# Kernel optimization log

Hardware: AMD Instinct MI355X
Metric: run time of the kernel (lower is better)

Reference implementation:

```python
import jax, jax.numpy as jnp
import numpy as np

B, H, L = 16, 1024, 4096


def setup_inputs() -> dict:
    key = jax.random.key(0)
    k1, k2 = jax.random.split(key)
    x = jax.random.normal(k1, (B, H, L), dtype=jnp.float32)
    # SSM kernel output k: (channels=1, d_model=H, L)
    k = jax.random.normal(k2, (1, H, L), dtype=jnp.float32) * 0.02
    D = jnp.ones((1, H, 1), dtype=jnp.float32)  # skip-connection scale
    return {"x": x, "k": k, "D": D}


def reference(x, k, D):
    # unidirectional FFT long convolution (S4-style):
    # y = irfft(rfft(x, 2L) * rfft(k, 2L))[..., :L] + x * D
    Lx = x.shape[-1]
    n = 2 * Lx
    k_f = jnp.fft.rfft(k, n=n)          # (1, H, n//2+1) complex
    x_f = jnp.fft.rfft(x, n=n)          # (B, H, n//2+1) complex
    y = jnp.fft.irfft(x_f * k_f, n=n)[..., :Lx]  # (B, H, L)
    return y + x * D
```

## Files before the change

### kernel.cpp

```cpp
#include <hip/hip_runtime.h>

#define LCONV 4096
#define NFFT 8192
#define NT 256
#define HCH 1024
#define BATCH 16
#define PI_F 3.14159265358979f
#define C707 0.70710678118654752f
#define C16A 0.92387953251128674f
#define S16A 0.38268343236508977f

#define SW(i) ((i) ^ (((i) >> 4) & 15))

__device__ __forceinline__ float2 cadd(float2 a, float2 b){ return make_float2(a.x+b.x, a.y+b.y); }
__device__ __forceinline__ float2 csub(float2 a, float2 b){ return make_float2(a.x-b.x, a.y-b.y); }
__device__ __forceinline__ float2 cmul(float2 a, float2 b){ return make_float2(a.x*b.x - a.y*b.y, a.x*b.y + a.y*b.x); }
__device__ __forceinline__ float2 mW81 (float2 d){ return make_float2( C707*(d.x+d.y),  C707*(d.y-d.x)); }
__device__ __forceinline__ float2 mNI  (float2 d){ return make_float2( d.y, -d.x); }
__device__ __forceinline__ float2 mW83 (float2 d){ return make_float2( C707*(d.y-d.x), -C707*(d.x+d.y)); }
__device__ __forceinline__ float2 mW81c(float2 d){ return make_float2( C707*(d.x-d.y),  C707*(d.x+d.y)); }
__device__ __forceinline__ float2 mPI  (float2 d){ return make_float2(-d.y,  d.x); }
__device__ __forceinline__ float2 mW83c(float2 d){ return make_float2(-C707*(d.x+d.y),  C707*(d.x-d.y)); }

__device__ __forceinline__ void net8_fwd(float2 a[8]) {
    float2 t0=cadd(a[0],a[4]), t4=csub(a[0],a[4]);
    float2 t1=cadd(a[1],a[5]), t5=mW81(csub(a[1],a[5]));
    float2 t2=cadd(a[2],a[6]), t6=mNI (csub(a[2],a[6]));
    float2 t3=cadd(a[3],a[7]), t7=mW83(csub(a[3],a[7]));
    float2 u0=cadd(t0,t2), u2=csub(t0,t2);
    float2 u1=cadd(t1,t3), u3=mNI(csub(t1,t3));
    float2 u4=cadd(t4,t6), u6=csub(t4,t6);
    float2 u5=cadd(t5,t7), u7=mNI(csub(t5,t7));
    a[0]=cadd(u0,u1); a[1]=csub(u0,u1);
    a[2]=cadd(u2,u3); a[3]=csub(u2,u3);
    a[4]=cadd(u4,u5); a[5]=csub(u4,u5);
    a[6]=cadd(u6,u7); a[7]=csub(u6,u7);
}
__device__ __forceinline__ void net8_inv(float2 a[8]) {
    float2 t0=cadd(a[0],a[4]), t4=csub(a[0],a[4]);
    float2 t1=cadd(a[1],a[5]), t5=mW81c(csub(a[1],a[5]));
    float2 t2=cadd(a[2],a[6]), t6=mPI  (csub(a[2],a[6]));
    float2 t3=cadd(a[3],a[7]), t7=mW83c(csub(a[3],a[7]));
    float2 u0=cadd(t0,t2), u2=csub(t0,t2);
    float2 u1=cadd(t1,t3), u3=mPI(csub(t1,t3));
    float2 u4=cadd(t4,t6), u6=csub(t4,t6);
    float2 u5=cadd(t5,t7), u7=mPI(csub(t5,t7));
    a[0]=cadd(u0,u1); a[1]=csub(u0,u1);
    a[2]=cadd(u2,u3); a[3]=csub(u2,u3);
    a[4]=cadd(u4,u5); a[5]=csub(u4,u5);
    a[6]=cadd(u6,u7); a[7]=csub(u6,u7);
}

template<int M, bool INV>
__device__ __forceinline__ void bf8(float2* z, int idx, const float2 w[8]) {
    float2 a[8];
    if (!INV) {
#pragma unroll
        for (int q = 0; q < 8; ++q) a[q] = z[SW(idx + q*M)];
        net8_fwd(a);
        z[SW(idx      )] = a[0];
        z[SW(idx + 4*M)] = cmul(a[1], w[4]);
        z[SW(idx + 2*M)] = cmul(a[2], w[2]);
        z[SW(idx + 6*M)] = cmul(a[3], w[6]);
        z[SW(idx + 1*M)] = cmul(a[4], w[1]);
        z[SW(idx + 5*M)] = cmul(a[5], w[5]);
        z[SW(idx + 3*M)] = cmul(a[6], w[3]);
        z[SW(idx + 7*M)] = cmul(a[7], w[7]);
    } else {
        a[0] = z[SW(idx)];
#pragma unroll
        for (int q = 1; q < 8; ++q) a[q] = cmul(z[SW(idx + q*M)], w[q]);
        net8_inv(a);
        z[SW(idx      )] = a[0];
        z[SW(idx + 4*M)] = a[1];
        z[SW(idx + 2*M)] = a[2];
        z[SW(idx + 6*M)] = a[3];
        z[SW(idx + 1*M)] = a[4];
        z[SW(idx + 5*M)] = a[5];
        z[SW(idx + 3*M)] = a[6];
        z[SW(idx + 7*M)] = a[7];
    }
}

template<int M, bool INV>
__device__ __forceinline__ void stage8(float2* z, int tid) {
    __syncthreads();
    const float ang = (INV ? 2.0f : -2.0f) * PI_F / (8.0f * (float)M);
    if (M == 1024) {
        float2 w1, wstep;
        __sincosf(ang * (float)tid, &w1.y, &w1.x);
        __sincosf(ang * 256.0f, &wstep.y, &wstep.x);
#pragma unroll
        for (int s = 0; s < 4; ++s) {
            float2 w[8];
            w[0] = make_float2(1.f, 0.f);
            w[1] = w1;
#pragma unroll
            for (int q = 2; q < 8; ++q) w[q] = cmul(w[q-1], w1);
            bf8<M, INV>(z, tid + 256*s, w);
            w1 = cmul(w1, wstep);
        }
    } else {
        const int LOG2M = (M == 128) ? 7 : 4;
        int j  = tid & (M - 1);
        int g0 = tid >> LOG2M;
        float2 w[8];
        w[0] = make_float2(1.f, 0.f);
        __sincosf(ang * (float)j, &w[1].y, &w[1].x);
#pragma unroll
        for (int q = 2; q < 8; ++q) w[q] = cmul(w[q-1], w[1]);
#pragma unroll
        for (int s = 0; s < 4; ++s) {
            int base = (g0 + (256 / M) * s) * (8 * M);
            bf8<M, INV>(z, base + j, w);
        }
    }
}

template<bool INV>
__device__ __forceinline__ void stage16(float2* z, int tid) {
    __syncthreads();
#pragma unroll
    for (int s = 0; s < 2; ++s) {
        int b = (tid + 256*s) * 16;
        float2 a[16];
#pragma unroll
        for (int e = 0; e < 16; ++e) a[e] = z[SW(b + e)];
        float2 lo[8], hi[8];
#pragma unroll
        for (int i = 0; i < 8; ++i) {
            lo[i] = cadd(a[i], a[i+8]);
            hi[i] = csub(a[i], a[i+8]);
        }
        if (!INV) {
            hi[1] = cmul(hi[1], make_float2( C16A, -S16A));
            hi[2] = mW81(hi[2]);
            hi[3] = cmul(hi[3], make_float2( S16A, -C16A));
            hi[4] = mNI (hi[4]);
            hi[5] = cmul(hi[5], make_float2(-S16A, -C16A));
            hi[6] = mW83(hi[6]);
            hi[7] = cmul(hi[7], make_float2(-C16A, -S16A));
            net8_fwd(lo); net8_fwd(hi);
        } else {
            hi[1] = cmul(hi[1], make_float2( C16A,  S16A));
            hi[2] = mW81c(hi[2]);
            hi[3] = cmul(hi[3], make_float2( S16A,  C16A));
            hi[4] = mPI (hi[4]);
            hi[5] = cmul(hi[5], make_float2(-S16A,  C16A));
            hi[6] = mW83c(hi[6]);
            hi[7] = cmul(hi[7], make_float2(-C16A,  S16A));
            net8_inv(lo); net8_inv(hi);
        }
        const int rev3[8] = {0,4,2,6,1,5,3,7};
#pragma unroll
        for (int s2 = 0; s2 < 8; ++s2) {
            z[SW(b + 2*rev3[s2]    )] = lo[s2];
            z[SW(b + 2*rev3[s2] + 1)] = hi[s2];
        }
    }
}

__global__ __launch_bounds__(NT) void kfft_kernel(const float* __restrict__ k,
                                                  float2* __restrict__ Kf) {
    __shared__ float2 z[NFFT];
    int h = blockIdx.x, tid = threadIdx.x;
    const float* kr = k + (size_t)h * LCONV;
#pragma unroll
    for (int jj = 0; jj < 16; ++jj) {
        int i = tid + NT*jj;
        z[SW(i)]         = make_float2(kr[i], 0.f);
        z[SW(i + LCONV)] = make_float2(0.f, 0.f);
    }
    stage8<1024, false>(z, tid);
    stage8<128,  false>(z, tid);
    stage8<16,   false>(z, tid);
    stage16<false>(z, tid);
    __syncthreads();
    const float invN = 1.0f / (float)NFFT;
    float2* out = Kf + (size_t)h * NFFT;
#pragma unroll
    for (int jj = 0; jj < 32; ++jj) {
        int i = tid + NT*jj;
        float2 v = z[SW(i)];
        out[i] = make_float2(v.x * invN, v.y * invN);
    }
}

__global__ __launch_bounds__(NT) void conv_kernel(const float* __restrict__ x,
                                                  const float2* __restrict__ Kf,
                                                  const float* __restrict__ Dv,
                                                  float* __restrict__ y) {
    __shared__ float2 z[NFFT];
    int bid = blockIdx.x;
    int h = bid >> 3;
    int pb = bid & 7;
    int b0 = pb*2, b1 = pb*2 + 1;
    int tid = threadIdx.x;

    const float* x0 = x + ((size_t)b0 * HCH + h) * LCONV;
    const float* x1 = x + ((size_t)b1 * HCH + h) * LCONV;

    float2 xr[16];
#pragma unroll
    for (int jj = 0; jj < 16; ++jj) {
        int i = tid + NT*jj;
        xr[jj] = make_float2(x0[i], x1[i]);
        z[SW(i)]         = xr[jj];
        z[SW(i + LCONV)] = make_float2(0.f, 0.f);
    }

    stage8<1024, false>(z, tid);
    stage8<128,  false>(z, tid);
    stage8<16,   false>(z, tid);
    stage16<false>(z, tid);

    __syncthreads();
    const float2* kf = Kf + (size_t)h * NFFT;
#pragma unroll
    for (int jj = 0; jj < 32; ++jj) {
        int i = tid + NT*jj;
        z[SW(i)] = cmul(z[SW(i)], kf[i]);
    }

    stage16<true>(z, tid);
    stage8<16,   true>(z, tid);
    stage8<128,  true>(z, tid);
    stage8<1024, true>(z, tid);

    __syncthreads();
    float d = Dv[h];
    float* y0 = y + ((size_t)b0 * HCH + h) * LCONV;
    float* y1 = y + ((size_t)b1 * HCH + h) * LCONV;
#pragma unroll
    for (int jj = 0; jj < 16; ++jj) {
        int i = tid + NT*jj;
        float2 r = z[SW(i)];
        y0[i] = r.x + xr[jj].x * d;
        y1[i] = r.y + xr[jj].y * d;
    }
}

extern "C" void kernel_launch(void* const* d_in, const int* in_sizes, int n_in,
                              void* d_out, int out_size, void* d_ws, size_t ws_size,
                              hipStream_t stream) {
    const float* x  = (const float*)d_in[0];
    const float* k  = (const float*)d_in[1];
    const float* Dv = (const float*)d_in[2];
    float* y  = (float*)d_out;
    float2* Kf = (float2*)d_ws;

    kfft_kernel<<<HCH, NT, 0, stream>>>(k, Kf);
    conv_kernel<<<HCH * (BATCH/2), NT, 0, stream>>>(x, Kf, Dv, y);
}
```

Baseline: 658.9 us.

## Restructure FFT convolution as 16x16x32 decomposition with fused skip term and pruned stages

```diff
diff --git a/kernel.cpp b/kernel.cpp
--- a/kernel.cpp
+++ b/kernel.cpp
@@ -1,28 +1,35 @@
 #include <hip/hip_runtime.h>
 
+
 #define LCONV 4096
-#define NFFT 8192
-#define NT 256
-#define HCH 1024
+#define NFFT  8192
+#define NT    256
+#define HCH   1024
 #define BATCH 16
-#define PI_F 3.14159265358979f
+
 #define C707 0.70710678118654752f
 #define C16A 0.92387953251128674f
 #define S16A 0.38268343236508977f
-
-#define SW(i) ((i) ^ (((i) >> 4) & 15))
-
-__device__ __forceinline__ float2 cadd(float2 a, float2 b){ return make_float2(a.x+b.x, a.y+b.y); }
-__device__ __forceinline__ float2 csub(float2 a, float2 b){ return make_float2(a.x-b.x, a.y-b.y); }
-__device__ __forceinline__ float2 cmul(float2 a, float2 b){ return make_float2(a.x*b.x - a.y*b.y, a.x*b.y + a.y*b.x); }
-__device__ __forceinline__ float2 mW81 (float2 d){ return make_float2( C707*(d.x+d.y),  C707*(d.y-d.x)); }
-__device__ __forceinline__ float2 mNI  (float2 d){ return make_float2( d.y, -d.x); }
-__device__ __forceinline__ float2 mW83 (float2 d){ return make_float2( C707*(d.y-d.x), -C707*(d.x+d.y)); }
-__device__ __forceinline__ float2 mW81c(float2 d){ return make_float2( C707*(d.x-d.y),  C707*(d.x+d.y)); }
-__device__ __forceinline__ float2 mPI  (float2 d){ return make_float2(-d.y,  d.x); }
-__device__ __forceinline__ float2 mW83c(float2 d){ return make_float2(-C707*(d.x+d.y),  C707*(d.x-d.y)); }
-
-__device__ __forceinline__ void net8_fwd(float2 a[8]) {
+#define C32A 0.98078528040323044f
+#define S32A 0.19509032201612827f
+#define C32B 0.83146961230254524f
+#define S32B 0.55557023301960222f
+
+#define A256f  (-0.0245436926061702596f)
+#define A512f  (-0.0122718463030851298f)
+#define A8192f (-7.66990393942820615e-4f)
+
+static __device__ __forceinline__ float2 cadd(float2 a, float2 b){ return make_float2(a.x+b.x, a.y+b.y); }
+static __device__ __forceinline__ float2 csub(float2 a, float2 b){ return make_float2(a.x-b.x, a.y-b.y); }
+static __device__ __forceinline__ float2 cmul(float2 a, float2 b){ return make_float2(a.x*b.x - a.y*b.y, a.x*b.y + a.y*b.x); }
+static __device__ __forceinline__ float2 mW81 (float2 d){ return make_float2( C707*(d.x+d.y),  C707*(d.y-d.x)); }
+static __device__ __forceinline__ float2 mNI  (float2 d){ return make_float2( d.y, -d.x); }
+static __device__ __forceinline__ float2 mW83 (float2 d){ return make_float2( C707*(d.y-d.x), -C707*(d.x+d.y)); }
+static __device__ __forceinline__ float2 mW81c(float2 d){ return make_float2( C707*(d.x-d.y),  C707*(d.x+d.y)); }
+static __device__ __forceinline__ float2 mPI  (float2 d){ return make_float2(-d.y,  d.x); }
+static __device__ __forceinline__ float2 mW83c(float2 d){ return make_float2(-C707*(d.x+d.y),  C707*(d.x-d.y)); }
+
+static __device__ __forceinline__ void net8_fwd(float2 a[8]) {
     float2 t0=cadd(a[0],a[4]), t4=csub(a[0],a[4]);
     float2 t1=cadd(a[1],a[5]), t5=mW81(csub(a[1],a[5]));
     float2 t2=cadd(a[2],a[6]), t6=mNI (csub(a[2],a[6]));
@@ -36,7 +43,7 @@
     a[4]=cadd(u4,u5); a[5]=csub(u4,u5);
     a[6]=cadd(u6,u7); a[7]=csub(u6,u7);
 }
-__device__ __forceinline__ void net8_inv(float2 a[8]) {
+static __device__ __forceinline__ void net8_inv(float2 a[8]) {
     float2 t0=cadd(a[0],a[4]), t4=csub(a[0],a[4]);
     float2 t1=cadd(a[1],a[5]), t5=mW81c(csub(a[1],a[5]));
     float2 t2=cadd(a[2],a[6]), t6=mPI  (csub(a[2],a[6]));
@@ -51,192 +58,340 @@
     a[6]=cadd(u6,u7); a[7]=csub(u6,u7);
 }
 
-template<int M, bool INV>
-__device__ __forceinline__ void bf8(float2* z, int idx, const float2 w[8]) {
-    float2 a[8];
-    if (!INV) {
-#pragma unroll
-        for (int q = 0; q < 8; ++q) a[q] = z[SW(idx + q*M)];
-        net8_fwd(a);
-        z[SW(idx      )] = a[0];
-        z[SW(idx + 4*M)] = cmul(a[1], w[4]);
-        z[SW(idx + 2*M)] = cmul(a[2], w[2]);
-        z[SW(idx + 6*M)] = cmul(a[3], w[6]);
-        z[SW(idx + 1*M)] = cmul(a[4], w[1]);
-        z[SW(idx + 5*M)] = cmul(a[5], w[5]);
-        z[SW(idx + 3*M)] = cmul(a[6], w[3]);
-        z[SW(idx + 7*M)] = cmul(a[7], w[7]);
-    } else {
-        a[0] = z[SW(idx)];
-#pragma unroll
-        for (int q = 1; q < 8; ++q) a[q] = cmul(z[SW(idx + q*M)], w[q]);
-        net8_inv(a);
-        z[SW(idx      )] = a[0];
-        z[SW(idx + 4*M)] = a[1];
-        z[SW(idx + 2*M)] = a[2];
-        z[SW(idx + 6*M)] = a[3];
-        z[SW(idx + 1*M)] = a[4];
-        z[SW(idx + 5*M)] = a[5];
-        z[SW(idx + 3*M)] = a[6];
-        z[SW(idx + 7*M)] = a[7];
-    }
-}
-
-template<int M, bool INV>
-__device__ __forceinline__ void stage8(float2* z, int tid) {
-    __syncthreads();
-    const float ang = (INV ? 2.0f : -2.0f) * PI_F / (8.0f * (float)M);
-    if (M == 1024) {
-        float2 w1, wstep;
-        __sincosf(ang * (float)tid, &w1.y, &w1.x);
-        __sincosf(ang * 256.0f, &wstep.y, &wstep.x);
-#pragma unroll
-        for (int s = 0; s < 4; ++s) {
-            float2 w[8];
-            w[0] = make_float2(1.f, 0.f);
-            w[1] = w1;
-#pragma unroll
-            for (int q = 2; q < 8; ++q) w[q] = cmul(w[q-1], w1);
-            bf8<M, INV>(z, tid + 256*s, w);
-            w1 = cmul(w1, wstep);
-        }
-    } else {
-        const int LOG2M = (M == 128) ? 7 : 4;
-        int j  = tid & (M - 1);
-        int g0 = tid >> LOG2M;
-        float2 w[8];
-        w[0] = make_float2(1.f, 0.f);
-        __sincosf(ang * (float)j, &w[1].y, &w[1].x);
-#pragma unroll
-        for (int q = 2; q < 8; ++q) w[q] = cmul(w[q-1], w[1]);
-#pragma unroll
-        for (int s = 0; s < 4; ++s) {
-            int base = (g0 + (256 / M) * s) * (8 * M);
-            bf8<M, INV>(z, base + j, w);
-        }
-    }
-}
-
-template<bool INV>
-__device__ __forceinline__ void stage16(float2* z, int tid) {
-    __syncthreads();
-#pragma unroll
-    for (int s = 0; s < 2; ++s) {
-        int b = (tid + 256*s) * 16;
-        float2 a[16];
-#pragma unroll
-        for (int e = 0; e < 16; ++e) a[e] = z[SW(b + e)];
-        float2 lo[8], hi[8];
-#pragma unroll
-        for (int i = 0; i < 8; ++i) {
-            lo[i] = cadd(a[i], a[i+8]);
-            hi[i] = csub(a[i], a[i+8]);
-        }
-        if (!INV) {
-            hi[1] = cmul(hi[1], make_float2( C16A, -S16A));
-            hi[2] = mW81(hi[2]);
-            hi[3] = cmul(hi[3], make_float2( S16A, -C16A));
-            hi[4] = mNI (hi[4]);
-            hi[5] = cmul(hi[5], make_float2(-S16A, -C16A));
-            hi[6] = mW83(hi[6]);
-            hi[7] = cmul(hi[7], make_float2(-C16A, -S16A));
-            net8_fwd(lo); net8_fwd(hi);
-        } else {
-            hi[1] = cmul(hi[1], make_float2( C16A,  S16A));
-            hi[2] = mW81c(hi[2]);
-            hi[3] = cmul(hi[3], make_float2( S16A,  C16A));
-            hi[4] = mPI (hi[4]);
-            hi[5] = cmul(hi[5], make_float2(-S16A,  C16A));
-            hi[6] = mW83c(hi[6]);
-            hi[7] = cmul(hi[7], make_float2(-C16A,  S16A));
-            net8_inv(lo); net8_inv(hi);
-        }
-        const int rev3[8] = {0,4,2,6,1,5,3,7};
-#pragma unroll
-        for (int s2 = 0; s2 < 8; ++s2) {
-            z[SW(b + 2*rev3[s2]    )] = lo[s2];
-            z[SW(b + 2*rev3[s2] + 1)] = hi[s2];
-        }
+static __device__ __forceinline__ void fft16_fwd(float2 a[16]) {
+    float2 lo[8], hi[8];
+#pragma unroll
+    for (int n=0;n<8;++n){ lo[n]=cadd(a[n],a[n+8]); hi[n]=csub(a[n],a[n+8]); }
+    hi[1]=cmul(hi[1],make_float2( C16A,-S16A));
+    hi[2]=mW81(hi[2]);
+    hi[3]=cmul(hi[3],make_float2( S16A,-C16A));
+    hi[4]=mNI(hi[4]);
+    hi[5]=cmul(hi[5],make_float2(-S16A,-C16A));
+    hi[6]=mW83(hi[6]);
+    hi[7]=cmul(hi[7],make_float2(-C16A,-S16A));
+    net8_fwd(lo); net8_fwd(hi);
+#pragma unroll
+    for (int s=0;s<8;++s){ a[s]=lo[s]; a[8+s]=hi[s]; }
+}
+static __device__ __forceinline__ void fft16_inv_nat(float2 a[16]) {
+    float2 lo[8], hi[8];
+#pragma unroll
+    for (int n=0;n<8;++n){ lo[n]=cadd(a[n],a[n+8]); hi[n]=csub(a[n],a[n+8]); }
+    hi[1]=cmul(hi[1],make_float2( C16A, S16A));
+    hi[2]=mW81c(hi[2]);
+    hi[3]=cmul(hi[3],make_float2( S16A, C16A));
+    hi[4]=mPI(hi[4]);
+    hi[5]=cmul(hi[5],make_float2(-S16A, C16A));
+    hi[6]=mW83c(hi[6]);
+    hi[7]=cmul(hi[7],make_float2(-C16A, S16A));
+    net8_inv(lo); net8_inv(hi);
+#pragma unroll
+    for (int s=0;s<8;++s){ a[s]=lo[s]; a[8+s]=hi[s]; }
+}
+static __device__ __forceinline__ void fft32_fwd(float2 a[32]) {
+    float2 lo[16], hi[16];
+#pragma unroll
+    for (int n=0;n<16;++n){ lo[n]=cadd(a[n],a[n+16]); hi[n]=csub(a[n],a[n+16]); }
+    hi[ 1]=cmul(hi[ 1],make_float2( C32A,-S32A));
+    hi[ 2]=cmul(hi[ 2],make_float2( C16A,-S16A));
+    hi[ 3]=cmul(hi[ 3],make_float2( C32B,-S32B));
+    hi[ 4]=mW81(hi[ 4]);
+    hi[ 5]=cmul(hi[ 5],make_float2( S32B,-C32B));
+    hi[ 6]=cmul(hi[ 6],make_float2( S16A,-C16A));
+    hi[ 7]=cmul(hi[ 7],make_float2( S32A,-C32A));
+    hi[ 8]=mNI(hi[ 8]);
+    hi[ 9]=cmul(hi[ 9],make_float2(-S32A,-C32A));
+    hi[10]=cmul(hi[10],make_float2(-S16A,-C16A));
+    hi[11]=cmul(hi[11],make_float2(-S32B,-C32B));
+    hi[12]=mW83(hi[12]);
+    hi[13]=cmul(hi[13],make_float2(-C32B,-S32B));
+    hi[14]=cmul(hi[14],make_float2(-C16A,-S16A));
+    hi[15]=cmul(hi[15],make_float2(-C32A,-S32A));
+    fft16_fwd(lo); fft16_fwd(hi);
+#pragma unroll
+    for (int s=0;s<16;++s){ a[s]=lo[s]; a[16+s]=hi[s]; }
+}
+
+static __device__ __forceinline__ void inv8_r2n(const float2 b[8], float2 o[8]) {
+    float2 e0=cadd(b[0],b[1]), e1=csub(b[0],b[1]);
+    float2 f0=cadd(b[2],b[3]), f1=mPI(csub(b[2],b[3]));
+    float2 E0=cadd(e0,f0), E2=csub(e0,f0);
+    float2 E1=cadd(e1,f1), E3=csub(e1,f1);
+    float2 g0=cadd(b[4],b[5]), g1=csub(b[4],b[5]);
+    float2 h0=cadd(b[6],b[7]), h1=mPI(csub(b[6],b[7]));
+    float2 O0=cadd(g0,h0), O2=csub(g0,h0);
+    float2 O1=cadd(g1,h1), O3=csub(g1,h1);
+    float2 T0=O0, T1=mW81c(O1), T2=mPI(O2), T3=mW83c(O3);
+    o[0]=cadd(E0,T0); o[4]=csub(E0,T0);
+    o[1]=cadd(E1,T1); o[5]=csub(E1,T1);
+    o[2]=cadd(E2,T2); o[6]=csub(E2,T2);
+    o[3]=cadd(E3,T3); o[7]=csub(E3,T3);
+}
+static __device__ __forceinline__ void inv16_r2n(const float2 a[16], float2 o[16]) {
+    float2 E[8], O[8];
+    inv8_r2n(a, E); inv8_r2n(a+8, O);
+    float2 T[8];
+    T[0]=O[0];
+    T[1]=cmul(O[1],make_float2( C16A, S16A));
+    T[2]=mW81c(O[2]);
+    T[3]=cmul(O[3],make_float2( S16A, C16A));
+    T[4]=mPI(O[4]);
+    T[5]=cmul(O[5],make_float2(-S16A, C16A));
+    T[6]=mW83c(O[6]);
+    T[7]=cmul(O[7],make_float2(-C16A, S16A));
+#pragma unroll
+    for (int n=0;n<8;++n){ o[n]=cadd(E[n],T[n]); o[n+8]=csub(E[n],T[n]); }
+}
+static __device__ __forceinline__ void inv32_r2n(const float2 a[32], float2 o[32]) {
+    float2 E[16], O[16], T;
+    inv16_r2n(a, E); inv16_r2n(a+16, O);
+    T=O[0];                                  o[ 0]=cadd(E[ 0],T); o[16]=csub(E[ 0],T);
+    T=cmul(O[ 1],make_float2( C32A, S32A)); o[ 1]=cadd(E[ 1],T); o[17]=csub(E[ 1],T);
+    T=cmul(O[ 2],make_float2( C16A, S16A)); o[ 2]=cadd(E[ 2],T); o[18]=csub(E[ 2],T);
+    T=cmul(O[ 3],make_float2( C32B, S32B)); o[ 3]=cadd(E[ 3],T); o[19]=csub(E[ 3],T);
+    T=mW81c(O[ 4]);                          o[ 4]=cadd(E[ 4],T); o[20]=csub(E[ 4],T);
+    T=cmul(O[ 5],make_float2( S32B, C32B)); o[ 5]=cadd(E[ 5],T); o[21]=csub(E[ 5],T);
+    T=cmul(O[ 6],make_float2( S16A, C16A)); o[ 6]=cadd(E[ 6],T); o[22]=csub(E[ 6],T);
+    T=cmul(O[ 7],make_float2( S32A, C32A)); o[ 7]=cadd(E[ 7],T); o[23]=csub(E[ 7],T);
+    T=mPI(O[ 8]);                            o[ 8]=cadd(E[ 8],T); o[24]=csub(E[ 8],T);
+    T=cmul(O[ 9],make_float2(-S32A, C32A)); o[ 9]=cadd(E[ 9],T); o[25]=csub(E[ 9],T);
+    T=cmul(O[10],make_float2(-S16A, C16A)); o[10]=cadd(E[10],T); o[26]=csub(E[10],T);
+    T=cmul(O[11],make_float2(-S32B, C32B)); o[11]=cadd(E[11],T); o[27]=csub(E[11],T);
+    T=mW83c(O[12]);                          o[12]=cadd(E[12],T); o[28]=csub(E[12],T);
+    T=cmul(O[13],make_float2(-C32B, S32B)); o[13]=cadd(E[13],T); o[29]=csub(E[13],T);
+    T=cmul(O[14],make_float2(-C16A, S16A)); o[14]=cadd(E[14],T); o[30]=csub(E[14],T);
+    T=cmul(O[15],make_float2(-C32A, S32A)); o[15]=cadd(E[15],T); o[31]=csub(E[15],T);
+}
+
+static __device__ __forceinline__ void f1_stage(float2* __restrict__ z, const float2 d[8],
+                                                int n2, int col)
+{
+    constexpr int rev3[8] = {0,4,2,6,1,5,3,7};
+    float2 lo[8], hi[8];
+    lo[0]=d[0]; hi[0]=d[0];
+    lo[1]=d[1]; hi[1]=cmul(d[1],make_float2( C16A,-S16A));
+    lo[2]=d[2]; hi[2]=mW81(d[2]);
+    lo[3]=d[3]; hi[3]=cmul(d[3],make_float2( S16A,-C16A));
+    lo[4]=d[4]; hi[4]=mNI(d[4]);
+    lo[5]=d[5]; hi[5]=cmul(d[5],make_float2(-S16A,-C16A));
+    lo[6]=d[6]; hi[6]=mW83(d[6]);
+    lo[7]=d[7]; hi[7]=cmul(d[7],make_float2(-C16A,-S16A));
+    net8_fwd(lo); net8_fwd(hi);
+    const float a1 = A256f * (float)n2;
+    float2 stp2; __sincosf(2.f*a1, &stp2.y, &stp2.x);
+    float2 ce = make_float2(1.f, 0.f);
+    float2 co; __sincosf(a1, &co.y, &co.x);
+#pragma unroll
+    for (int m=0;m<8;++m){
+        if (m==4){ __sincosf(8.f*a1, &ce.y, &ce.x); __sincosf(9.f*a1, &co.y, &co.x); }
+        const int s2 = rev3[m];
+        z[512*(2*m)   + col] = cmul(lo[s2], ce);
+        z[512*(2*m+1) + col] = cmul(hi[s2], co);
+        ce = cmul(ce, stp2); co = cmul(co, stp2);
+    }
+}
+
+static __device__ __forceinline__ void f2_write(float2* __restrict__ z, const float2 a[16],
+                                                int k1, int n3)
+{
+    constexpr int K16[16]={0,8,4,12,2,10,6,14,1,9,5,13,3,11,7,15};
+    const float ab = A8192f * (float)(n3*k1);
+    const float as = A512f  * (float)n3;
+    float2 stp; __sincosf(as, &stp.y, &stp.x);
+    float2 cur; __sincosf(ab, &cur.y, &cur.x);
+    const int wb = 512*k1 + (n3 ^ k1);
+#pragma unroll
+    for (int j=0;j<16;++j){
+        if (j==8) __sincosf(ab + 8.f*as, &cur.y, &cur.x);
+        z[wb + 32*j] = cmul(a[K16[j]], cur);
+        cur = cmul(cur, stp);
+    }
+}
+
+static __device__ __forceinline__ void f2i_write(float2* __restrict__ z, const float2 a[16],
+                                                 int k1, int n3)
+{
+    constexpr int K16[16]={0,8,4,12,2,10,6,14,1,9,5,13,3,11,7,15};
+    const float ab = -A8192f * (float)(n3*k1);
+    const float as = -A256f  * (float)k1;
+    float2 stp; __sincosf(as, &stp.y, &stp.x);
+    float2 cur; __sincosf(ab, &cur.y, &cur.x);
+    const int wb = 512*k1 + n3;
+#pragma unroll
+    for (int j=0;j<16;++j){
+        if (j==8) __sincosf(ab + 8.f*as, &cur.y, &cur.x);
+        z[wb + 32*j] = cmul(a[K16[j]], cur);
+        cur = cmul(cur, stp);
     }
 }
 
 __global__ __launch_bounds__(NT) void kfft_kernel(const float* __restrict__ k,
-                                                  float2* __restrict__ Kf) {
+                                                  float2* __restrict__ Kf)
+{
     __shared__ float2 z[NFFT];
-    int h = blockIdx.x, tid = threadIdx.x;
-    const float* kr = k + (size_t)h * LCONV;
-#pragma unroll
-    for (int jj = 0; jj < 16; ++jj) {
-        int i = tid + NT*jj;
-        z[SW(i)]         = make_float2(kr[i], 0.f);
-        z[SW(i + LCONV)] = make_float2(0.f, 0.f);
-    }
-    stage8<1024, false>(z, tid);
-    stage8<128,  false>(z, tid);
-    stage8<16,   false>(z, tid);
-    stage16<false>(z, tid);
-    __syncthreads();
-    const float invN = 1.0f / (float)NFFT;
-    float2* out = Kf + (size_t)h * NFFT;
-#pragma unroll
-    for (int jj = 0; jj < 32; ++jj) {
-        int i = tid + NT*jj;
-        float2 v = z[SW(i)];
-        out[i] = make_float2(v.x * invN, v.y * invN);
+    const int h = blockIdx.x, t = threadIdx.x;
+    const int n3 = t & 31, g = t >> 5;
+    const float* __restrict__ kr = k + (size_t)h * LCONV;
+
+#pragma unroll
+    for (int s=0;s<2;++s){
+        const int n2 = 2*g + s;
+        const int col = 32*n2 + n3;
+        float2 d[8];
+#pragma unroll
+        for (int n=0;n<8;++n) d[n] = make_float2(kr[512*n + col], 0.f);
+        f1_stage(z, d, n2, col);
+    }
+    __syncthreads();
+
+    float2 a0[16], a1[16];
+    {
+        const int b0 = 512*(2*g) + n3, b1 = b0 + 512;
+#pragma unroll
+        for (int n=0;n<16;++n) a0[n] = z[b0 + 32*n];
+#pragma unroll
+        for (int n=0;n<16;++n) a1[n] = z[b1 + 32*n];
+    }
+    fft16_fwd(a0); fft16_fwd(a1);
+    __syncthreads();
+    f2_write(z, a0, 2*g,   n3);
+    f2_write(z, a1, 2*g+1, n3);
+    __syncthreads();
+
+    {
+        const int k1 = t & 15, k2 = t >> 4;
+        const int vx = 513*k1 + 32*k2;
+        float2 b[32];
+#pragma unroll
+        for (int q=0;q<32;++q) b[q] = z[vx ^ q];
+        fft32_fwd(b);
+        float2* __restrict__ op = Kf + (size_t)h*NFFT + t;
+        const float sc = 1.0f/(float)NFFT;
+#pragma unroll
+        for (int q=0;q<32;++q)
+            op[256*q] = make_float2(b[q].x*sc, b[q].y*sc);
     }
 }
 
 __global__ __launch_bounds__(NT) void conv_kernel(const float* __restrict__ x,
                                                   const float2* __restrict__ Kf,
                                                   const float* __restrict__ Dv,
-                                                  float* __restrict__ y) {
+                                                  float* __restrict__ y)
+{
     __shared__ float2 z[NFFT];
-    int bid = blockIdx.x;
-    int h = bid >> 3;
-    int pb = bid & 7;
-    int b0 = pb*2, b1 = pb*2 + 1;
-    int tid = threadIdx.x;
-
-    const float* x0 = x + ((size_t)b0 * HCH + h) * LCONV;
-    const float* x1 = x + ((size_t)b1 * HCH + h) * LCONV;
-
-    float2 xr[16];
-#pragma unroll
-    for (int jj = 0; jj < 16; ++jj) {
-        int i = tid + NT*jj;
-        xr[jj] = make_float2(x0[i], x1[i]);
-        z[SW(i)]         = xr[jj];
-        z[SW(i + LCONV)] = make_float2(0.f, 0.f);
-    }
-
-    stage8<1024, false>(z, tid);
-    stage8<128,  false>(z, tid);
-    stage8<16,   false>(z, tid);
-    stage16<false>(z, tid);
-
-    __syncthreads();
-    const float2* kf = Kf + (size_t)h * NFFT;
-#pragma unroll
-    for (int jj = 0; jj < 32; ++jj) {
-        int i = tid + NT*jj;
-        z[SW(i)] = cmul(z[SW(i)], kf[i]);
-    }
-
-    stage16<true>(z, tid);
-    stage8<16,   true>(z, tid);
-    stage8<128,  true>(z, tid);
-    stage8<1024, true>(z, tid);
-
-    __syncthreads();
-    float d = Dv[h];
-    float* y0 = y + ((size_t)b0 * HCH + h) * LCONV;
-    float* y1 = y + ((size_t)b1 * HCH + h) * LCONV;
-#pragma unroll
-    for (int jj = 0; jj < 16; ++jj) {
-        int i = tid + NT*jj;
-        float2 r = z[SW(i)];
-        y0[i] = r.x + xr[jj].x * d;
-        y1[i] = r.y + xr[jj].y * d;
+    constexpr int rev3[8]={0,4,2,6,1,5,3,7};
+
+    const int bid = blockIdx.x;
+    const int r  = bid & 7;
+    const int jj = bid >> 3;
+    const int h  = r*(HCH/8) + (jj >> 3);
+    const int pb = jj & 7;
+    const int t  = threadIdx.x;
+    const int n3 = t & 31, g = t >> 5;
+
+    const float* __restrict__ x0 = x + ((size_t)(2*pb  )*HCH + h)*LCONV;
+    const float* __restrict__ x1 = x + ((size_t)(2*pb+1)*HCH + h)*LCONV;
+
+#pragma unroll
+    for (int s=0;s<2;++s){
+        const int n2 = 2*g + s;
+        const int col = 32*n2 + n3;
+        float2 d[8];
+#pragma unroll
+        for (int n=0;n<8;++n)
+            d[n] = make_float2(x0[512*n + col], x1[512*n + col]);
+        f1_stage(z, d, n2, col);
+    }
+    __syncthreads();
+
+    float2 a0[16], a1[16];
+    {
+        const int b0 = 512*(2*g) + n3, b1 = b0 + 512;
+#pragma unroll
+        for (int n=0;n<16;++n) a0[n] = z[b0 + 32*n];
+#pragma unroll
+        for (int n=0;n<16;++n) a1[n] = z[b1 + 32*n];
+    }
+    fft16_fwd(a0); fft16_fwd(a1);
+    __syncthreads();
+    f2_write(z, a0, 2*g,   n3);
+    f2_write(z, a1, 2*g+1, n3);
+    __syncthreads();
+
+    {
+        const int k1 = t & 15, k2 = t >> 4;
+        const float2* __restrict__ kfp = Kf + (size_t)h*NFFT + t;
+        float2 kf[32];
+#pragma unroll
+        for (int q=0;q<32;++q) kf[q] = kfp[256*q];
+        const float dN = Dv[h] * (1.0f/(float)NFFT);
+        const int vx = 513*k1 + 32*k2;
+        float2 b[32];
+#pragma unroll
+        for (int q=0;q<32;++q) b[q] = z[vx ^ q];
+        fft32_fwd(b);
+#pragma unroll
+        for (int q=0;q<32;++q)
+            b[q] = cmul(b[q], make_float2(kf[q].x + dN, kf[q].y));
+        float2 c[32];
+        inv32_r2n(b, c);
+        const float as = -A512f * (float)k2;
+        float2 stp; __sincosf(as, &stp.y, &stp.x);
+        float2 cur = make_float2(1.f, 0.f);
+#pragma unroll
+        for (int q=0;q<32;++q){
+            if (q && (q&7)==0) __sincosf(as*(float)q, &cur.y, &cur.x);
+            z[vx ^ q] = cmul(c[q], cur);
+            cur = cmul(cur, stp);
+        }
+    }
+    __syncthreads();
+
+    {
+        const int k1a = 2*g, k1b = 2*g+1;
+        const int b0 = 512*k1a + (n3 ^ k1a);
+        const int b1 = 512*k1b + (n3 ^ k1b);
+#pragma unroll
+        for (int n=0;n<16;++n) a0[n] = z[b0 + 32*n];
+#pragma unroll
+        for (int n=0;n<16;++n) a1[n] = z[b1 + 32*n];
+    }
+    fft16_inv_nat(a0); fft16_inv_nat(a1);
+    __syncthreads();
+    f2i_write(z, a0, 2*g,   n3);
+    f2i_write(z, a1, 2*g+1, n3);
+    __syncthreads();
+
+    float* __restrict__ y0 = y + ((size_t)(2*pb  )*HCH + h)*LCONV;
+    float* __restrict__ y1 = y + ((size_t)(2*pb+1)*HCH + h)*LCONV;
+#pragma unroll
+    for (int s=0;s<2;++s){
+        const int n2 = 2*g + s;
+        const int col = 32*n2 + n3;
+        float2 ev[8], od[8];
+#pragma unroll
+        for (int m=0;m<8;++m){
+            ev[m] = z[512*(2*m)   + col];
+            od[m] = z[512*(2*m+1) + col];
+        }
+        net8_inv(ev); net8_inv(od);
+#pragma unroll
+        for (int n1=0;n1<8;++n1){
+            float2 E  = ev[rev3[n1]];
+            float2 Ov = od[rev3[n1]];
+            float2 T;
+            if      (n1==0) T = Ov;
+            else if (n1==1) T = cmul(Ov, make_float2( C16A, S16A));
+            else if (n1==2) T = mW81c(Ov);
+            else if (n1==3) T = cmul(Ov, make_float2( S16A, C16A));
+            else if (n1==4) T = mPI(Ov);
+            else if (n1==5) T = cmul(Ov, make_float2(-S16A, C16A));
+            else if (n1==6) T = mW83c(Ov);
+            else            T = cmul(Ov, make_float2(-C16A, S16A));
+            float2 o = cadd(E, T);
+            y0[512*n1 + col] = o.x;
+            y1[512*n1 + col] = o.y;
+        }
     }
 }
 
@@ -246,7 +401,7 @@
     const float* x  = (const float*)d_in[0];
     const float* k  = (const float*)d_in[1];
     const float* Dv = (const float*)d_in[2];
-    float* y  = (float*)d_out;
+    float* y   = (float*)d_out;
     float2* Kf = (float2*)d_ws;
 
     kfft_kernel<<<HCH, NT, 0, stream>>>(k, Kf);
```

After: 725.1 us. +10.0%, slower.
